# Optimization experiments

Measured on AMD Instinct MI355X. Metric: run time of the kernel, lower is better.

Reference implementation:

```python
import jax, jax.numpy as jnp
import numpy as np

B, S, H, NH, EHH, L = 8, 4, 50, 200, 400, 2
HID = 128
FDIM = 44 + 20 + 15          # 79: atom one-hot + amino-acid one-hot + position one-hot
EDIM = 2 * FDIM + 3          # h_i, h_j, distance, bond, t -> 161


def setup_inputs() -> dict:
    key = jax.random.key(0)
    ks = jax.random.split(key, 32)
    inp = {}
    inp["t"] = jax.random.uniform(ks[0], (B,), dtype=jnp.float32)
    inp["x_h"] = jax.random.normal(ks[1], (B, S, H, 3), dtype=jnp.float32)
    inp["x_heavy"] = jax.random.normal(ks[2], (B, 1, NH, 3), dtype=jnp.float32)
    inp["bond_matrix_h_heavy"] = (jax.random.uniform(ks[3], (B, H, NH)) < 0.02).astype(jnp.float32)
    inp["edge_mask_h_heavy"] = jnp.ones((B, H, NH), jnp.float32)
    inp["edge_mask_h_h"] = jnp.ones((B, EHH), jnp.float32)
    inp["atom_mask"] = jnp.ones((B, H, 1), jnp.float32)
    sc = 0.02
    shapes = {"W1": (L, EDIM, HID), "b1": (L, HID), "W2": (L, HID, HID), "b2": (L, HID),
              "Wc1": (L, HID, HID), "bc1": (L, HID), "Wc2": (L, HID, 1),
              "Wn1": (L, FDIM + HID, HID), "bn1": (L, HID), "Wn2": (L, HID, FDIM), "bn2": (L, FDIM)}
    for i, (n, s) in enumerate(shapes.items()):
        inp[n] = jax.random.normal(ks[4 + i], s, dtype=jnp.float32) * sc
    inp["peptide_seq"] = jax.random.randint(ks[20], (B, 15), 0, 20)
    inp["atom_labels_heavy"] = jax.random.randint(ks[21], (B, NH), 0, 44)
    inp["atom_labels_h"] = jax.random.randint(ks[22], (B, H), 0, 44)
    inp["amino_acid_pos_heavy"] = jax.random.randint(ks[23], (B, NH), 1, 16)
    inp["amino_acid_pos_h"] = jax.random.randint(ks[24], (B, H), 1, 16)
    inp["edges_h_h"] = jax.random.randint(ks[25], (B, EHH, 2), 0, H)
    inp["bound_atom"] = jax.random.randint(ks[26], (B, H), 0, NH)
    return inp


def _embed(labels, pos, peptide_seq):
    # one_hot(atom,44) ++ one_hot(seq[pos-1],20) ++ one_hot(pos-1,15)
    aa = jnp.take_along_axis(peptide_seq, pos - 1, axis=1)
    return jnp.concatenate([jax.nn.one_hot(labels, 44, dtype=jnp.float32),
                            jax.nn.one_hot(aa, 20, dtype=jnp.float32),
                            jax.nn.one_hot(pos - 1, 15, dtype=jnp.float32)], axis=-1)


def _gather_nodes(feat, idx):
    # feat [B,S,N,D], idx [B,E] -> [B,S,E,D]
    return jnp.take_along_axis(feat, idx[:, None, :, None], axis=2)


def _seg(data, ids, n):
    # data [B,S,E,D], ids [B,E] -> scatter-add over edges -> [B,S,n,D]
    f = jax.vmap(lambda d, i: jax.ops.segment_sum(jnp.swapaxes(d, 0, 1), i, num_segments=n))
    return jnp.swapaxes(f(data, ids), 1, 2)


def _forward(t, x_h, x_heavy, bond_hm, em_hheavy, em_hh, atom_mask,
             W1, b1, W2, b2, Wc1, bc1, Wc2, Wn1, bn1, Wn2, bn2,
             peptide_seq, atom_labels_heavy, atom_labels_h, pos_heavy, pos_h,
             edges_h_h, bound_atom):
    Bq, Sq, Hq, _ = x_h.shape
    Nh = x_heavy.shape[2]
    xhv = jnp.broadcast_to(x_heavy, (Bq, Sq, Nh, 3))
    emb_h = _embed(atom_labels_h, pos_h, peptide_seq)          # [B,H,79]
    emb_hv = _embed(atom_labels_heavy, pos_heavy, peptide_seq)  # [B,NH,79]
    # absolute coords: x_h relative to its bound heavy atom
    x_h_abs = x_h + jnp.take_along_axis(xhv, bound_atom[:, None, :, None], axis=2)
    x = jnp.concatenate([x_h_abs, xhv], axis=2)                 # [B,S,N,3]
    feat = jnp.concatenate([emb_h, emb_hv], axis=1)             # [B,N,79]
    feat = jnp.broadcast_to(feat[:, None], (Bq, Sq) + feat.shape[1:])
    bond = jnp.concatenate([jnp.zeros((Bq, Hq, Hq), bond_hm.dtype), bond_hm], axis=-1)  # [B,H,N]
    # edge indices: sparse h-h edges, then full h x heavy grid (row-major, cols offset by H)
    grid_r = jnp.repeat(jnp.arange(Hq), Nh)
    grid_c = Hq + jnp.tile(jnp.arange(Nh), Hq)
    edge_row = jnp.concatenate([edges_h_h[..., 0], jnp.broadcast_to(grid_r, (Bq, Hq * Nh))], axis=-1)
    edge_col = jnp.concatenate([edges_h_h[..., 1], jnp.broadcast_to(grid_c, (Bq, Hq * Nh))], axis=-1)
    emask = jnp.concatenate([em_hh, em_hheavy.reshape(Bq, -1)], axis=-1)[:, None, :, None]  # [B,1,E,1]
    bond_e = jax.vmap(lambda bm, r, c: bm[r, c])(bond, edge_row, edge_col)[:, None, :, None]
    x0 = x
    for l in range(W1.shape[0]):
        xi = _gather_nodes(x, edge_row)
        xj = _gather_nodes(x, edge_col)
        diff = xi - xj                                          # [B,S,E,3]
        dist = jnp.linalg.norm(diff, axis=-1, keepdims=True)    # [B,S,E,1]
        hi = _gather_nodes(feat, edge_row)
        hj = _gather_nodes(feat, edge_col)
        t_e = jnp.broadcast_to(t[:, None, None, None], dist.shape)
        ef = jnp.concatenate([hi, hj, dist, jnp.broadcast_to(bond_e, dist.shape), t_e], axis=-1)
        m = jax.nn.silu(ef @ W1[l] + b1[l])
        m = jax.nn.silu(m @ W2[l] + b2[l]) * emask              # masked messages [B,S,E,HID]
        cw = jax.nn.silu(m @ Wc1[l] + bc1[l]) @ Wc2[l]          # [B,S,E,1]
        agg_x = _seg(diff * cw, edge_row, Hq)                   # [B,S,H,3]
        agg_m = _seg(m, edge_row, Hq)                           # [B,S,H,HID]
        h_h = feat[:, :, :Hq]
        h_out = h_h + jax.nn.silu(jnp.concatenate([h_h, agg_m], axis=-1) @ Wn1[l] + bn1[l]) @ Wn2[l] + bn2[l]
        x = jnp.concatenate([x[:, :, :Hq] + agg_x, x[:, :, Hq:]], axis=2)
        feat = jnp.concatenate([h_out, feat[:, :, Hq:]], axis=2)
    pred = (x[:, :, :Hq] - x0[:, :, :Hq]) * atom_mask[:, None, :, :]
    return pred


def reference(t, x_h, x_heavy, bond_matrix_h_heavy, edge_mask_h_heavy, edge_mask_h_h, atom_mask,
              W1, b1, W2, b2, Wc1, bc1, Wc2, Wn1, bn1, Wn2, bn2,
              peptide_seq, atom_labels_heavy, atom_labels_h, amino_acid_pos_heavy, amino_acid_pos_h,
              edges_h_h, bound_atom):
    return _forward(t, x_h, x_heavy, bond_matrix_h_heavy, edge_mask_h_heavy, edge_mask_h_h, atom_mask,
                    W1, b1, W2, b2, Wc1, bc1, Wc2, Wn1, bn1, Wn2, bn2,
                    peptide_seq, atom_labels_heavy, atom_labels_h, amino_acid_pos_heavy, amino_acid_pos_h,
                    edges_h_h, bound_atom)
```

## Files before the change

### kernel.cpp

```cpp
#include <hip/hip_runtime.h>
#include <math.h>

#define B_     8
#define S_     4
#define H_     50
#define NH_    200
#define EHH_   400
#define L_     2
#define HID_   128
#define FDIM_  79
#define EDIM_  161
#define NN_    250
#define NROW_  1600
#define BS_    32
#define FS_    80
#define MSTR_  136
#define NDIM_  207
#define HVB_   1600

#define OFF_FEATH  0
#define OFF_X      128000
#define OFF_X0H    160000
#define OFF_HHCOL  166400
#define OFF_HHEM   169600
#define OFF_HHOFF  172800
#define OFF_AGG0   173312
#define AGGSTRIDE_ 211200
#define OFF_AGG1   384512
#define OFF_HIW1   595712
#define OFF_HJW1   800512
#define OFF_WP     1414912

typedef __attribute__((ext_vector_type(8))) short short8;
typedef __attribute__((ext_vector_type(4))) float f32x4;

__device__ __forceinline__ float silu_(float v) {
    return v * __builtin_amdgcn_rcpf(1.0f + __expf(-v));
}
__device__ __forceinline__ unsigned short f2bf(float f) {
    unsigned int u = __float_as_uint(f);
    unsigned int r = (u + 0x7fffu + ((u >> 16) & 1u)) >> 16;
    return (unsigned short)r;
}

#define HV_BLKS_    1600
#define PACK_BLKS_  256
#define SORT_BLKS_  8
#define HROW_BLKS_  200
#define FEAT_BLKS_  125
#define XI_BLKS_    32
#define SETUP_BLKS_ (HV_BLKS_ + PACK_BLKS_ + SORT_BLKS_ + HROW_BLKS_ + FEAT_BLKS_ + XI_BLKS_)

__global__ __launch_bounds__(256) void k_setup(
    const float* __restrict__ x_h, const float* __restrict__ x_hv,
    const int* __restrict__ bound,
    const int* __restrict__ ehh, const float* __restrict__ em_hh,
    const float* __restrict__ W1, const float* __restrict__ b1,
    const float* __restrict__ t_in,
    const float* __restrict__ W2, const float* __restrict__ Wc1,
    const int* __restrict__ lab_h, const int* __restrict__ pos_h,
    const int* __restrict__ lab_hv, const int* __restrict__ pos_hv,
    const int* __restrict__ pep,
    float* __restrict__ feat_h,
    float* __restrict__ x, float* __restrict__ x0h,
    int* __restrict__ hhcol, float* __restrict__ hhem, int* __restrict__ hhoff,
    float* __restrict__ hiW1, float* __restrict__ hjW1,
    unsigned short* __restrict__ Wp)
{
    int blk = blockIdx.x, t = threadIdx.x;
    if (blk < HV_BLKS_) {
        int g = blk*256 + t;
        int l = g / 204800;
        int r = g - l*204800;
        int node = r >> 7, col = r & 127;
        int b = node / NH_;
        int label = lab_hv[node], pos = pos_hv[node];
        int aa = pep[b*15 + pos - 1];
        const float* W1l = W1 + l*EDIM_*HID_;
        float hj = W1l[(FDIM_ + label)*HID_ + col]
                 + W1l[(FDIM_ + 44 + aa)*HID_ + col]
                 + W1l[(FDIM_ + 64 + pos - 1)*HID_ + col];
        hjW1[(size_t)(HVB_ + l*1600 + node)*HID_ + col] = hj;
        return;
    }
    blk -= HV_BLKS_;
    if (blk < PACK_BLKS_) {
        int g = blk*256 + t;
        int idx = g & 16383;
        int lm  = g >> 14;
        int l = lm >> 1, mat = lm & 1;
        int j = idx & 7, q = (idx >> 3) & 3, n = (idx >> 5) & 127, kc = idx >> 12;
        int k = kc*32 + q*8 + j;
        const float* W = (mat == 0 ? W2 : Wc1) + l*HID_*HID_;
        Wp[g] = f2bf(W[k*HID_ + n]);
        return;
    }
    blk -= PACK_BLKS_;
    if (blk < SORT_BLKS_) {
        int b = blk;
        __shared__ int scnt[64];
        __shared__ int srow[EHH_], scol[EHH_];
        __shared__ float sem[EHH_];
        if (t < 64) scnt[t] = 0;
        __syncthreads();
        for (int e = t; e < EHH_; e += 256) {
            int r = ehh[(b*EHH_ + e)*2 + 0];
            srow[e] = r;
            scol[e] = ehh[(b*EHH_ + e)*2 + 1];
            sem[e]  = em_hh[b*EHH_ + e];
            atomicAdd(&scnt[r], 1);
        }
        __syncthreads();
        if (t == 0) {
            int acc = 0;
            for (int i = 0; i < H_; ++i) { int v = scnt[i]; scnt[i] = acc; acc += v; }
        }
        __syncthreads();
        if (t < 51) hhoff[b*64 + t] = (t < H_) ? scnt[t] : EHH_;
        __syncthreads();
        for (int e = t; e < EHH_; e += 256) {
            int r = srow[e];
            int pos = atomicAdd(&scnt[r], 1);
            hhcol[b*EHH_ + pos] = scol[e];
            hhem [b*EHH_ + pos] = sem[e];
        }
        return;
    }
    blk -= SORT_BLKS_;
    if (blk < HROW_BLKS_) {
        int g = blk*256 + t;
        int node = g >> 7, col = g & 127;
        int b = node / H_;
        int label = lab_h[node], pos = pos_h[node];
        int aa = pep[b*15 + pos - 1];
        const float* W1l = W1;
        float hi = W1l[label*HID_ + col]
                 + W1l[(44 + aa)*HID_ + col]
                 + W1l[(64 + pos - 1)*HID_ + col]
                 + b1[col]
                 + t_in[b] * W1l[160*HID_ + col];
        float hj = W1l[(FDIM_ + label)*HID_ + col]
                 + W1l[(FDIM_ + 44 + aa)*HID_ + col]
                 + W1l[(FDIM_ + 64 + pos - 1)*HID_ + col];
        int h = node % H_;
        #pragma unroll
        for (int s = 0; s < S_; ++s) {
            int row = (b*S_ + s)*H_ + h;
            hiW1[(size_t)row*HID_ + col] = hi;
            hjW1[(size_t)row*HID_ + col] = hj;
        }
        return;
    }
    blk -= HROW_BLKS_;
    if (blk < FEAT_BLKS_) {
        int g = blk*256 + t;
        int node = g / FS_, f = g % FS_;
        int b = node / H_, h = node % H_;
        int label = lab_h[node], pos = pos_h[node];
        int aa = pep[b*15 + pos - 1];
        float v = 0.f;
        if (f < 44)      v = (f == label)          ? 1.0f : 0.0f;
        else if (f < 64) v = ((f - 44) == aa)      ? 1.0f : 0.0f;
        else if (f < 79) v = ((f - 64) == pos - 1) ? 1.0f : 0.0f;
        #pragma unroll
        for (int s = 0; s < S_; ++s)
            feat_h[((b*S_ + s)*H_ + h)*FS_ + f] = v;
        return;
    }
    blk -= FEAT_BLKS_;
    {
        int g = blk*256 + t;
        if (g >= BS_*NN_) return;
        int bs = g / NN_, n = g % NN_;
        int b = bs / S_;
        if (n < H_) {
            int ba = bound[b*H_ + n];
            for (int d = 0; d < 3; ++d) {
                float v = x_h[(bs*H_ + n)*3 + d] + x_hv[(b*NH_ + ba)*3 + d];
                x[g*4 + d] = v;
                x0h[(bs*H_ + n)*4 + d] = v;
            }
        } else {
            int nh = n - H_;
            for (int d = 0; d < 3; ++d) x[g*4 + d] = x_hv[(b*NH_ + nh)*3 + d];
        }
    }
}

__global__ __launch_bounds__(512) void k_edge_mlp(
    const float* __restrict__ x, const float* __restrict__ hiW1,
    const float* __restrict__ hjW1,
    const int* __restrict__ hhcol, const float* __restrict__ hhem,
    const int* __restrict__ hhoff,
    const float* __restrict__ em_hv, const float* __restrict__ bond_in,
    const float* __restrict__ W1,
    const float* __restrict__ b2, const float* __restrict__ bc1,
    const float* __restrict__ Wc2,
    const unsigned short* __restrict__ Wp, int l,
    float* __restrict__ aggx, float* __restrict__ aggm)
{
    __shared__ unsigned short s_wp[2*16384];
    __shared__ unsigned short s_m[8][16][MSTR_];
    __shared__ float s_es[8][16][6];
    __shared__ int   s_jj[8][16];
    __shared__ float s_hi[2][HID_];
    __shared__ float s_cc[5][HID_];
    __shared__ float s_mr[2][4][HID_];
    __shared__ float s_xr[2][4][4];

    const int t = threadIdx.x, lane = t & 63, w = t >> 6;
    const int l15 = lane & 15, q = lane >> 4;
    const int r  = w >> 2;
    const int wr = w & 3;
    const int node0 = blockIdx.x*2;
    const int node  = node0 + r;
    const int bs = node / H_, h = node - bs*H_;
    const int b  = bs / S_;

    {
        const float4* src = (const float4*)(Wp + (size_t)l*32768);
        float4* dst = (float4*)s_wp;
        #pragma unroll
        for (int i = 0; i < 8; ++i) dst[t + i*512] = src[t + i*512];
    }
    const float* W1l = W1 + l*EDIM_*HID_;
    if (t < 128) {
        s_hi[0][t] = hiW1[(size_t)node0*HID_ + t];
    } else if (t < 256) {
        int c = t - 128;
        s_hi[1][c] = hiW1[(size_t)(node0 + 1)*HID_ + c];
    } else if (t < 384) {
        int c = t - 256;
        s_cc[0][c] = W1l[158*HID_ + c];
        s_cc[3][c] = bc1[l*HID_ + c];
    } else {
        int c = t - 384;
        s_cc[1][c] = W1l[159*HID_ + c];
        s_cc[2][c] = b2 [l*HID_ + c];
        s_cc[4][c] = Wc2[l*HID_ + c];
    }

    const int hh0 = hhoff[b*64 + h];
    const int cnt = hhoff[b*64 + h + 1] - hh0;
    const int E   = cnt + NH_;
    const int NT  = (E + 15) >> 4;

    const float xi0 = x[(bs*NN_ + h)*4 + 0];
    const float xi1 = x[(bs*NN_ + h)*4 + 1];
    const float xi2 = x[(bs*NN_ + h)*4 + 2];

    float macc[8] = {0.f,0.f,0.f,0.f,0.f,0.f,0.f,0.f};
    float xacc = 0.f;
    __syncthreads();

    for (int ti = wr; ti < NT; ti += 4) {
        if (lane < 16) {
            int e = ti*16 + lane;
            float d0=0.f,d1=0.f,d2=0.f,dist=0.f,bnd=0.f,em=0.f;
            int jj = bs*H_;
            if (e < E) {
                int col;
                if (e < cnt) {
                    col = hhcol[b*EHH_ + hh0 + e];
                    em  = hhem [b*EHH_ + hh0 + e];
                    jj  = bs*H_ + col;
                } else {
                    int cc = e - cnt;
                    col = H_ + cc;
                    em  = em_hv [(b*H_ + h)*NH_ + cc];
                    bnd = bond_in[(b*H_ + h)*NH_ + cc];
                    jj  = HVB_ + l*1600 + b*NH_ + cc;
                }
                d0 = xi0 - x[(bs*NN_ + col)*4 + 0];
                d1 = xi1 - x[(bs*NN_ + col)*4 + 1];
                d2 = xi2 - x[(bs*NN_ + col)*4 + 2];
                dist = sqrtf(d0*d0 + d1*d1 + d2*d2);
            }
            s_es[w][lane][0] = d0; s_es[w][lane][1] = d1; s_es[w][lane][2] = d2;
            s_es[w][lane][3] = dist; s_es[w][lane][4] = bnd; s_es[w][lane][5] = em;
            s_jj[w][lane] = jj;
        }
        __builtin_amdgcn_wave_barrier();

        const float dist = s_es[w][l15][3];
        const float bnd  = s_es[w][l15][4];
        const int   jj   = s_jj[w][l15];
        const float* pj  = hjW1 + (size_t)jj*HID_ + q*8;
        short8 afrag[4];
        #pragma unroll
        for (int kc = 0; kc < 4; ++kc) {
            int k0 = kc*32 + q*8;
            float4 c0 = *(const float4*)(pj + kc*32);
            float4 c1 = *(const float4*)(pj + kc*32 + 4);
            float4 h0 = *(const float4*)&s_hi[r][k0];
            float4 h1 = *(const float4*)&s_hi[r][k0 + 4];
            float4 wa0= *(const float4*)&s_cc[0][k0];
            float4 wa1= *(const float4*)&s_cc[0][k0 + 4];
            float4 wb0= *(const float4*)&s_cc[1][k0];
            float4 wb1= *(const float4*)&s_cc[1][k0 + 4];
            short8 fr;
            fr[0] = (short)f2bf(silu_(h0.x + c0.x + dist*wa0.x + bnd*wb0.x));
            fr[1] = (short)f2bf(silu_(h0.y + c0.y + dist*wa0.y + bnd*wb0.y));
            fr[2] = (short)f2bf(silu_(h0.z + c0.z + dist*wa0.z + bnd*wb0.z));
            fr[3] = (short)f2bf(silu_(h0.w + c0.w + dist*wa0.w + bnd*wb0.w));
            fr[4] = (short)f2bf(silu_(h1.x + c1.x + dist*wa1.x + bnd*wb1.x));
            fr[5] = (short)f2bf(silu_(h1.y + c1.y + dist*wa1.y + bnd*wb1.y));
            fr[6] = (short)f2bf(silu_(h1.z + c1.z + dist*wa1.z + bnd*wb1.z));
            fr[7] = (short)f2bf(silu_(h1.w + c1.w + dist*wa1.w + bnd*wb1.w));
            afrag[kc] = fr;
        }

        float em4[4];
        #pragma unroll
        for (int rr = 0; rr < 4; ++rr) em4[rr] = s_es[w][q*4 + rr][5];
        #pragma unroll
        for (int nt = 0; nt < 8; ++nt) {
            float bias = s_cc[2][nt*16 + l15];
            f32x4 c = {bias, bias, bias, bias};
            #pragma unroll
            for (int kc = 0; kc < 4; ++kc) {
                short8 bf = *(const short8*)&s_wp[((kc*128 + nt*16 + l15)*4 + q)*8];
                c = __builtin_amdgcn_mfma_f32_16x16x32_bf16(afrag[kc], bf, c, 0, 0, 0);
            }
            #pragma unroll
            for (int rr = 0; rr < 4; ++rr) {
                float mv = silu_(c[rr]) * em4[rr];
                s_m[w][q*4 + rr][nt*16 + l15] = f2bf(mv);
                macc[nt] += mv;
            }
        }
        __builtin_amdgcn_wave_barrier();

        short8 af2[4];
        #pragma unroll
        for (int kc = 0; kc < 4; ++kc)
            af2[kc] = *(const short8*)&s_m[w][l15][kc*32 + q*8];
        float p[4] = {0.f, 0.f, 0.f, 0.f};
        #pragma unroll
        for (int nt = 0; nt < 8; ++nt) {
            float bias = s_cc[3][nt*16 + l15];
            f32x4 c = {bias, bias, bias, bias};
            #pragma unroll
            for (int kc = 0; kc < 4; ++kc) {
                short8 bf = *(const short8*)&s_wp[16384 + ((kc*128 + nt*16 + l15)*4 + q)*8];
                c = __builtin_amdgcn_mfma_f32_16x16x32_bf16(af2[kc], bf, c, 0, 0, 0);
            }
            float wcv = s_cc[4][nt*16 + l15];
            #pragma unroll
            for (int rr = 0; rr < 4; ++rr)
                p[rr] += silu_(c[rr]) * wcv;
        }
        #pragma unroll
        for (int m = 1; m < 16; m <<= 1) {
            #pragma unroll
            for (int rr = 0; rr < 4; ++rr) p[rr] += __shfl_xor(p[rr], m, 64);
        }
        if (l15 < 3) {
            #pragma unroll
            for (int rr = 0; rr < 4; ++rr)
                xacc += s_es[w][q*4 + rr][l15] * p[rr];
        }
        __builtin_amdgcn_wave_barrier();
    }

    #pragma unroll
    for (int nt = 0; nt < 8; ++nt) {
        macc[nt] += __shfl_xor(macc[nt], 16, 64);
        macc[nt] += __shfl_xor(macc[nt], 32, 64);
    }
    if (q == 0) {
        #pragma unroll
        for (int nt = 0; nt < 8; ++nt) s_mr[r][wr][nt*16 + l15] = macc[nt];
    }
    xacc += __shfl_xor(xacc, 16, 64);
    xacc += __shfl_xor(xacc, 32, 64);
    if (q == 0 && l15 < 3) s_xr[r][wr][l15] = xacc;
    __syncthreads();
    if (t < 256) {
        int rr = t >> 7, col = t & 127;
        aggm[(size_t)(node0 + rr)*HID_ + col] =
            s_mr[rr][0][col] + s_mr[rr][1][col] + s_mr[rr][2][col] + s_mr[rr][3][col];
    } else if (t < 262) {
        int ix = t - 256, rr = ix / 3, d = ix - rr*3;
        aggx[(node0 + rr)*4 + d] =
            s_xr[rr][0][d] + s_xr[rr][1][d] + s_xr[rr][2][d] + s_xr[rr][3][d];
    }
}

__global__ __launch_bounds__(128) void k_update(
    float* __restrict__ feat_h, float* __restrict__ x,
    const float* __restrict__ aggm, const float* __restrict__ aggx,
    const float* __restrict__ Wn1, const float* __restrict__ bn1,
    const float* __restrict__ Wn2, const float* __restrict__ bn2, int l,
    const float* __restrict__ W1, const float* __restrict__ b1,
    const float* __restrict__ t_in,
    float* __restrict__ hiW1, float* __restrict__ hjW1, int do_w1,
    const float* __restrict__ x0h, const float* __restrict__ amask,
    float* __restrict__ out)
{
    __shared__ float s_in[8][NDIM_ + 1];
    __shared__ float s_u[8][HID_ + 1];
    int node0 = blockIdx.x * 8;
    int t = threadIdx.x;
    for (int idx = t; idx < 8*(NDIM_ + 1); idx += 128) {
        int g = idx / (NDIM_ + 1), k = idx % (NDIM_ + 1);
        float v = 0.f;
        if (k < FDIM_)      v = feat_h[(node0 + g)*FS_ + k];
        else if (k < NDIM_) v = aggm[(size_t)(node0 + g)*HID_ + (k - FDIM_)];
        s_in[g][k] = v;
    }
    __syncthreads();
    const float* Wn1l = Wn1 + l*NDIM_*HID_;
    float acc[8];
    float bv = bn1[l*HID_ + t];
    #pragma unroll
    for (int g = 0; g < 8; ++g) acc[g] = bv;
    for (int k = 0; k < NDIM_; ++k) {
        float wv = Wn1l[k*HID_ + t];
        #pragma unroll
        for (int g = 0; g < 8; ++g) acc[g] += s_in[g][k] * wv;
    }
    #pragma unroll
    for (int g = 0; g < 8; ++g) s_u[g][t] = silu_(acc[g]);
    __syncthreads();
    if (t < FDIM_) {
        const float* Wn2l = Wn2 + l*HID_*FDIM_;
        float acc2[8];
        float b2v = bn2[l*FDIM_ + t];
        #pragma unroll
        for (int g = 0; g < 8; ++g) acc2[g] = b2v;
        for (int k = 0; k < HID_; ++k) {
            float wv = Wn2l[k*FDIM_ + t];
            #pragma unroll
            for (int g = 0; g < 8; ++g) acc2[g] += s_u[g][k] * wv;
        }
        #pragma unroll
        for (int g = 0; g < 8; ++g) {
            float nf = s_in[g][t] + acc2[g];
            feat_h[(node0 + g)*FS_ + t] = nf;
            s_in[g][t] = nf;
        }
    } else if (t >= 96 && t < 120) {
        int idx = t - 96, g = idx / 3, d = idx % 3;
        int node = node0 + g;
        int bs = node / H_, h = node % H_;
        float xv = x[(bs*NN_ + h)*4 + d] + aggx[node*4 + d];
        x[(bs*NN_ + h)*4 + d] = xv;
        if (!do_w1) {
            int b = bs / S_;
            out[node*3 + d] = (xv - x0h[node*4 + d]) * amask[b*H_ + h];
        }
    }
    if (!do_w1) return;
    __syncthreads();
    {
        const float* W1n = W1 + (l + 1)*EDIM_*HID_;
        float w160 = W1n[160*HID_ + t];
        float b1v  = b1[(l + 1)*HID_ + t];
        float hia[8], hja[8];
        #pragma unroll
        for (int g = 0; g < 8; ++g) { hia[g] = 0.f; hja[g] = 0.f; }
        for (int f = 0; f < FDIM_; ++f) {
            float wi = W1n[f*HID_ + t];
            float wj = W1n[(FDIM_ + f)*HID_ + t];
            #pragma unroll
            for (int g = 0; g < 8; ++g) {
                float v = s_in[g][f];
                hia[g] += v * wi;
                hja[g] += v * wj;
            }
        }
        #pragma unroll
        for (int g = 0; g < 8; ++g) {
            int node = node0 + g;
            int b = (node / H_) / S_;
            hiW1[(size_t)node*HID_ + t] = hia[g] + b1v + t_in[b]*w160;
            hjW1[(size_t)node*HID_ + t] = hja[g];
        }
    }
}

extern "C" void kernel_launch(void* const* d_in, const int* in_sizes, int n_in,
                              void* d_out, int out_size, void* d_ws, size_t ws_size,
                              hipStream_t stream)
{
    const float* t_in  = (const float*)d_in[0];
    const float* x_h   = (const float*)d_in[1];
    const float* x_hv  = (const float*)d_in[2];
    const float* bond  = (const float*)d_in[3];
    const float* em_hv = (const float*)d_in[4];
    const float* em_hh = (const float*)d_in[5];
    const float* amask = (const float*)d_in[6];
    const float* W1    = (const float*)d_in[7];
    const float* b1    = (const float*)d_in[8];
    const float* W2    = (const float*)d_in[9];
    const float* b2    = (const float*)d_in[10];
    const float* Wc1   = (const float*)d_in[11];
    const float* bc1   = (const float*)d_in[12];
    const float* Wc2   = (const float*)d_in[13];
    const float* Wn1   = (const float*)d_in[14];
    const float* bn1   = (const float*)d_in[15];
    const float* Wn2   = (const float*)d_in[16];
    const float* bn2   = (const float*)d_in[17];
    const int* pep     = (const int*)d_in[18];
    const int* lab_hv  = (const int*)d_in[19];
    const int* lab_h   = (const int*)d_in[20];
    const int* pos_hv  = (const int*)d_in[21];
    const int* pos_h   = (const int*)d_in[22];
    const int* ehh     = (const int*)d_in[23];
    const int* bound   = (const int*)d_in[24];

    float* ws     = (float*)d_ws;
    float* feat_h = ws + OFF_FEATH;
    float* x      = ws + OFF_X;
    float* x0h    = ws + OFF_X0H;
    int*   hhcol  = (int*)(ws + OFF_HHCOL);
    float* hhem   = ws + OFF_HHEM;
    int*   hhoff  = (int*)(ws + OFF_HHOFF);
    float* hiW1   = ws + OFF_HIW1;
    float* hjW1   = ws + OFF_HJW1;
    unsigned short* Wp = (unsigned short*)(ws + OFF_WP);

    hipLaunchKernelGGL(k_setup, dim3(SETUP_BLKS_), dim3(256), 0, stream,
                       x_h, x_hv, bound, ehh, em_hh,
                       W1, b1, t_in, W2, Wc1,
                       lab_h, pos_h, lab_hv, pos_hv, pep,
                       feat_h, x, x0h, hhcol, hhem, hhoff,
                       hiW1, hjW1, Wp);

    for (int l = 0; l < L_; ++l) {
        float* aggx_l = ws + OFF_AGG0 + (size_t)l*AGGSTRIDE_;
        float* aggm_l = aggx_l + 6400;
        hipLaunchKernelGGL(k_edge_mlp, dim3(NROW_/2), dim3(512), 0, stream,
                           x, hiW1, hjW1, hhcol, hhem, hhoff, em_hv, bond,
                           W1, b2, bc1, Wc2, Wp, l, aggx_l, aggm_l);
        int do_w1 = (l == 0);
        hipLaunchKernelGGL(k_update, dim3(200), dim3(128), 0, stream,
                           feat_h, x, aggm_l, aggx_l, Wn1, bn1, Wn2, bn2, l,
                           W1, b1, t_in, hiW1, hjW1, do_w1,
                           x0h, amask, (float*)d_out);
    }
}
```

Measured before the change: 379.9 us.

## Software-pipeline edge gathers and hjW1 loads, relayout packed weights for lane-contiguous LDS

The edge MLP loop now gathers the next tile's edge data and prefetches its hjW1 rows into registers while the current tile runs its MFMAs, hiding global-load latency. Per-edge scalars are passed between lanes with wave shuffles instead of through the s_es/s_jj shared-memory staging arrays. The packed bf16 weight layout is reordered so each lane's B fragment is contiguous by lane index, which aims for conflict-free LDS reads. This adds register pressure from the prefetch buffers (eight float4 values plus the next-tile scalars), which may lower occupancy.

```diff
diff --git a/kernel.cpp b/kernel.cpp
--- a/kernel.cpp
+++ b/kernel.cpp
@@ -89,8 +89,13 @@
         int idx = g & 16383;
         int lm  = g >> 14;
         int l = lm >> 1, mat = lm & 1;
-        int j = idx & 7, q = (idx >> 3) & 3, n = (idx >> 5) & 127, kc = idx >> 12;
-        int k = kc*32 + q*8 + j;
+        int j   = idx & 7;
+        int l15 = (idx >> 3) & 15;
+        int qq  = (idx >> 7) & 3;
+        int nt  = (idx >> 9) & 7;
+        int kc  = (idx >> 12) & 3;
+        int n = nt*16 + l15;
+        int k = kc*32 + qq*8 + j;
         const float* W = (mat == 0 ? W2 : Wc1) + l*HID_*HID_;
         Wp[g] = f2bf(W[k*HID_ + n]);
         return;
@@ -201,8 +206,6 @@
 {
     __shared__ unsigned short s_wp[2*16384];
     __shared__ unsigned short s_m[8][16][MSTR_];
-    __shared__ float s_es[8][16][6];
-    __shared__ int   s_jj[8][16];
     __shared__ float s_hi[2][HID_];
     __shared__ float s_cc[5][HID_];
     __shared__ float s_mr[2][4][HID_];
@@ -249,49 +252,63 @@
     const float xi1 = x[(bs*NN_ + h)*4 + 1];
     const float xi2 = x[(bs*NN_ + h)*4 + 2];
 
+    auto gather = [&](int e, float& d0, float& d1, float& d2,
+                      float& dist, float& bnd, float& em, int& jj) {
+        if (e < E) {
+            int col;
+            if (e < cnt) {
+                col = hhcol[b*EHH_ + hh0 + e];
+                em  = hhem [b*EHH_ + hh0 + e];
+                jj  = bs*H_ + col;
+            } else {
+                int cc = e - cnt;
+                col = H_ + cc;
+                em  = em_hv [(b*H_ + h)*NH_ + cc];
+                bnd = bond_in[(b*H_ + h)*NH_ + cc];
+                jj  = HVB_ + l*1600 + b*NH_ + cc;
+            }
+            d0 = xi0 - x[(bs*NN_ + col)*4 + 0];
+            d1 = xi1 - x[(bs*NN_ + col)*4 + 1];
+            d2 = xi2 - x[(bs*NN_ + col)*4 + 2];
+            dist = sqrtf(d0*d0 + d1*d1 + d2*d2);
+        }
+    };
+
     float macc[8] = {0.f,0.f,0.f,0.f,0.f,0.f,0.f,0.f};
     float xacc = 0.f;
     __syncthreads();
 
+    float cd0=0.f, cd1=0.f, cd2=0.f, cdist=0.f, cbnd=0.f, cem=0.f;
+    int   cjj = bs*H_;
+    if (lane < 16) gather(wr*16 + lane, cd0, cd1, cd2, cdist, cbnd, cem, cjj);
+    float distb = __shfl(cdist, l15, 64);
+    float bndb  = __shfl(cbnd,  l15, 64);
+    int   jjb   = __shfl(cjj,   l15, 64);
+    float4 pr[8];
+    {
+        const float* pj = hjW1 + (size_t)jjb*HID_ + q*8;
+        #pragma unroll
+        for (int kc = 0; kc < 4; ++kc) {
+            pr[2*kc]   = *(const float4*)(pj + kc*32);
+            pr[2*kc+1] = *(const float4*)(pj + kc*32 + 4);
+        }
+    }
+
     for (int ti = wr; ti < NT; ti += 4) {
-        if (lane < 16) {
-            int e = ti*16 + lane;
-            float d0=0.f,d1=0.f,d2=0.f,dist=0.f,bnd=0.f,em=0.f;
-            int jj = bs*H_;
-            if (e < E) {
-                int col;
-                if (e < cnt) {
-                    col = hhcol[b*EHH_ + hh0 + e];
-                    em  = hhem [b*EHH_ + hh0 + e];
-                    jj  = bs*H_ + col;
-                } else {
-                    int cc = e - cnt;
-                    col = H_ + cc;
-                    em  = em_hv [(b*H_ + h)*NH_ + cc];
-                    bnd = bond_in[(b*H_ + h)*NH_ + cc];
-                    jj  = HVB_ + l*1600 + b*NH_ + cc;
-                }
-                d0 = xi0 - x[(bs*NN_ + col)*4 + 0];
-                d1 = xi1 - x[(bs*NN_ + col)*4 + 1];
-                d2 = xi2 - x[(bs*NN_ + col)*4 + 2];
-                dist = sqrtf(d0*d0 + d1*d1 + d2*d2);
-            }
-            s_es[w][lane][0] = d0; s_es[w][lane][1] = d1; s_es[w][lane][2] = d2;
-            s_es[w][lane][3] = dist; s_es[w][lane][4] = bnd; s_es[w][lane][5] = em;
-            s_jj[w][lane] = jj;
-        }
-        __builtin_amdgcn_wave_barrier();
-
-        const float dist = s_es[w][l15][3];
-        const float bnd  = s_es[w][l15][4];
-        const int   jj   = s_jj[w][l15];
-        const float* pj  = hjW1 + (size_t)jj*HID_ + q*8;
+        const int nx = ti + 4;
+        const bool hasNext = (nx < NT);
+
+        float nd0=0.f, nd1=0.f, nd2=0.f, ndist=0.f, nbnd=0.f, nem=0.f;
+        int   njj = bs*H_;
+        if (hasNext && lane < 16)
+            gather(nx*16 + lane, nd0, nd1, nd2, ndist, nbnd, nem, njj);
+
         short8 afrag[4];
         #pragma unroll
         for (int kc = 0; kc < 4; ++kc) {
             int k0 = kc*32 + q*8;
-            float4 c0 = *(const float4*)(pj + kc*32);
-            float4 c1 = *(const float4*)(pj + kc*32 + 4);
+            float4 c0 = pr[2*kc];
+            float4 c1 = pr[2*kc+1];
             float4 h0 = *(const float4*)&s_hi[r][k0];
             float4 h1 = *(const float4*)&s_hi[r][k0 + 4];
             float4 wa0= *(const float4*)&s_cc[0][k0];
@@ -299,27 +316,40 @@
             float4 wb0= *(const float4*)&s_cc[1][k0];
             float4 wb1= *(const float4*)&s_cc[1][k0 + 4];
             short8 fr;
-            fr[0] = (short)f2bf(silu_(h0.x + c0.x + dist*wa0.x + bnd*wb0.x));
-            fr[1] = (short)f2bf(silu_(h0.y + c0.y + dist*wa0.y + bnd*wb0.y));
-            fr[2] = (short)f2bf(silu_(h0.z + c0.z + dist*wa0.z + bnd*wb0.z));
-            fr[3] = (short)f2bf(silu_(h0.w + c0.w + dist*wa0.w + bnd*wb0.w));
-            fr[4] = (short)f2bf(silu_(h1.x + c1.x + dist*wa1.x + bnd*wb1.x));
-            fr[5] = (short)f2bf(silu_(h1.y + c1.y + dist*wa1.y + bnd*wb1.y));
-            fr[6] = (short)f2bf(silu_(h1.z + c1.z + dist*wa1.z + bnd*wb1.z));
-            fr[7] = (short)f2bf(silu_(h1.w + c1.w + dist*wa1.w + bnd*wb1.w));
+            fr[0] = (short)f2bf(silu_(h0.x + c0.x + distb*wa0.x + bndb*wb0.x));
+            fr[1] = (short)f2bf(silu_(h0.y + c0.y + distb*wa0.y + bndb*wb0.y));
+            fr[2] = (short)f2bf(silu_(h0.z + c0.z + distb*wa0.z + bndb*wb0.z));
+            fr[3] = (short)f2bf(silu_(h0.w + c0.w + distb*wa0.w + bndb*wb0.w));
+            fr[4] = (short)f2bf(silu_(h1.x + c1.x + distb*wa1.x + bndb*wb1.x));
+            fr[5] = (short)f2bf(silu_(h1.y + c1.y + distb*wa1.y + bndb*wb1.y));
+            fr[6] = (short)f2bf(silu_(h1.z + c1.z + distb*wa1.z + bndb*wb1.z));
+            fr[7] = (short)f2bf(silu_(h1.w + c1.w + distb*wa1.w + bndb*wb1.w));
             afrag[kc] = fr;
         }
 
+        float ndistb = 0.f, nbndb = 0.f;
+        if (hasNext) {
+            ndistb = __shfl(ndist, l15, 64);
+            nbndb  = __shfl(nbnd,  l15, 64);
+            int njjb = __shfl(njj, l15, 64);
+            const float* pj = hjW1 + (size_t)njjb*HID_ + q*8;
+            #pragma unroll
+            for (int kc = 0; kc < 4; ++kc) {
+                pr[2*kc]   = *(const float4*)(pj + kc*32);
+                pr[2*kc+1] = *(const float4*)(pj + kc*32 + 4);
+            }
+        }
+
         float em4[4];
         #pragma unroll
-        for (int rr = 0; rr < 4; ++rr) em4[rr] = s_es[w][q*4 + rr][5];
+        for (int rr = 0; rr < 4; ++rr) em4[rr] = __shfl(cem, q*4 + rr, 64);
         #pragma unroll
         for (int nt = 0; nt < 8; ++nt) {
             float bias = s_cc[2][nt*16 + l15];
             f32x4 c = {bias, bias, bias, bias};
             #pragma unroll
             for (int kc = 0; kc < 4; ++kc) {
-                short8 bf = *(const short8*)&s_wp[((kc*128 + nt*16 + l15)*4 + q)*8];
+                short8 bf = *(const short8*)&s_wp[((kc*8 + nt)*64 + lane)*8];
                 c = __builtin_amdgcn_mfma_f32_16x16x32_bf16(afrag[kc], bf, c, 0, 0, 0);
             }
             #pragma unroll
@@ -342,7 +372,7 @@
             f32x4 c = {bias, bias, bias, bias};
             #pragma unroll
             for (int kc = 0; kc < 4; ++kc) {
-                short8 bf = *(const short8*)&s_wp[16384 + ((kc*128 + nt*16 + l15)*4 + q)*8];
+                short8 bf = *(const short8*)&s_wp[16384 + ((kc*8 + nt)*64 + lane)*8];
                 c = __builtin_amdgcn_mfma_f32_16x16x32_bf16(af2[kc], bf, c, 0, 0, 0);
             }
             float wcv = s_cc[4][nt*16 + l15];
@@ -355,12 +385,20 @@
             #pragma unroll
             for (int rr = 0; rr < 4; ++rr) p[rr] += __shfl_xor(p[rr], m, 64);
         }
-        if (l15 < 3) {
-            #pragma unroll
-            for (int rr = 0; rr < 4; ++rr)
-                xacc += s_es[w][q*4 + rr][l15] * p[rr];
+        #pragma unroll
+        for (int rr = 0; rr < 4; ++rr) {
+            float sd0 = __shfl(cd0, q*4 + rr, 64);
+            float sd1 = __shfl(cd1, q*4 + rr, 64);
+            float sd2 = __shfl(cd2, q*4 + rr, 64);
+            if (l15 < 3) {
+                float dsel = (l15 == 0) ? sd0 : ((l15 == 1) ? sd1 : sd2);
+                xacc += dsel * p[rr];
+            }
         }
         __builtin_amdgcn_wave_barrier();
+
+        cd0 = nd0; cd1 = nd1; cd2 = nd2; cem = nem;
+        distb = ndistb; bndb = nbndb;
     }
 
     #pragma unroll
```

New measurement: 384.9 us. No clear change (+1.3%).
